# Optimization experiments

Hardware: AMD Instinct MI355X
Metric: run time of the kernel (lower is better)

The kernel has to match this reference:

```python
import jax, jax.numpy as jnp
import numpy as np

EPS = 1e-8  # smoothing_radius


def setup_inputs() -> dict:
    key = jax.random.key(0)
    ks = jax.random.split(key, 8)
    T, S, D = 2048, 1024, 3
    H, FIN, FOUT = 64, 7, 4
    return {
        "reference_length": jnp.ones((), jnp.float32),
        "source_points": jax.random.normal(ks[0], (S, D), jnp.float32),
        "target_points": jax.random.normal(ks[1], (T, D), jnp.float32),
        "source_strengths": jax.random.uniform(ks[2], (S,), jnp.float32),
        "source_area": jax.random.uniform(ks[3], (S,), jnp.float32),
        "source_normal": jax.random.normal(ks[4], (S, D), jnp.float32),
        "W1": jax.random.normal(ks[5], (FIN, H), jnp.float32) / np.sqrt(FIN),
        "b1": jnp.zeros((H,), jnp.float32),
        "W2": jax.random.normal(ks[6], (H, FOUT), jnp.float32) / np.sqrt(H),
        "b2": jnp.zeros((FOUT,), jnp.float32),
    }


def _legendre4(x):
    # First 4 Legendre polynomials P1..P4 (n_spherical_harmonics = 4)
    x2 = x * x
    p1 = x
    p2 = 0.5 * (3.0 * x2 - 1.0)
    p3 = 0.5 * (5.0 * x2 - 3.0) * x
    p4 = 0.125 * ((35.0 * x2 - 30.0) * x2 + 3.0)
    return jnp.stack([p1, p2, p3, p4], axis=-1)


def _kernel_forward(reference_length, source_points, target_points,
                    source_strengths, source_area, source_normal,
                    W1, b1, W2, b2):
    D = source_points.shape[-1]
    # Dimensionless relative positions: [T, S, D]
    r = (target_points[:, None, :] - source_points[None, :, :]) / reference_length
    r2 = jnp.sum(r * r, axis=-1) + EPS * EPS          # [T, S]
    n2 = jnp.sum(source_normal * source_normal, -1) + EPS * EPS  # [S]
    # Invariant features: source scalar, smoothed log-magnitudes, pair Legendre terms
    log_r = 0.5 * jnp.log(r2)                          # [T, S]
    log_n = 0.5 * jnp.log(n2)                          # [S]
    cos = jnp.einsum('tsd,sd->ts', r, source_normal) / jnp.sqrt(r2 * n2[None, :])
    feats = jnp.concatenate([
        jnp.broadcast_to(source_area[None, :, None], r2.shape + (1,)),
        log_r[..., None],
        jnp.broadcast_to(log_n[None, :, None], r2.shape + (1,)),
        _legendre4(cos),
    ], axis=-1)                                        # [T, S, 7]
    # MLP kernel network with tanh squashing (network_type='mlp')
    h = jax.nn.silu(feats @ W1 + b1)                   # [T, S, 64]
    out = jnp.tanh(h @ W2 + b2)                        # [T, S, 4]
    # Physical far-field decay: scalar ~ 1/r^{D-2}, vector ~ 1/r^{D-1}
    inv_r = jax.lax.rsqrt(r2)
    decay_s = inv_r ** (D - 2)
    decay_v = inv_r ** (D - 1)
    w = source_strengths[None, :]                      # [1, S]
    scalar = jnp.sum(w * decay_s * out[..., 0], axis=-1)  # [T]
    # Rotationally invariant vector reprojection: radial + 2 coeffs per non-radial vector
    r_hat = r * inv_r[..., None]
    n_hat = source_normal / jnp.sqrt(n2)[:, None]
    n_hat_b = jnp.broadcast_to(n_hat[None], r.shape)
    vec = (out[..., 1:2] * r_hat
           + out[..., 2:3] * n_hat_b
           + out[..., 3:4] * jnp.cross(r_hat, n_hat_b))  # [T, S, D]
    vector = jnp.einsum('ts,tsd->td', w * decay_v, vec)   # [T, D]
    return jnp.concatenate([scalar[:, None], vector], axis=-1)  # [T, 1+D]


def reference(reference_length, source_points, target_points, source_strengths,
              source_area, source_normal, W1, b1, W2, b2):
    return _kernel_forward(reference_length, source_points, target_points,
                           source_strengths, source_area, source_normal,
                           W1, b1, W2, b2)
```

## Files before the change

### kernel.cpp

```cpp
#include <hip/hip_runtime.h>

#define EPS2 1e-16f

constexpr int H      = 64;
constexpr int PBLOCK = 256;
constexpr int BLOCK  = 256;
constexpr int NCHUNK = 4;
constexpr float LOG2E = 1.4426950408889634f;

__device__ __forceinline__ float rcpf_fast(float x) { return __builtin_amdgcn_rcpf(x); }
__device__ __forceinline__ float rsqf_fast(float x) { return __builtin_amdgcn_rsqf(x); }
__device__ __forceinline__ float exp2_fast(float x) { return __builtin_amdgcn_exp2f(x); }

__global__ void prep(const float* __restrict__ refLenP,
                     const float* __restrict__ srcP,
                     const float* __restrict__ srcN,
                     const float* __restrict__ wgtP,
                     const float* __restrict__ areaP,
                     const float* __restrict__ W1,
                     const float* __restrict__ b1,
                     const float* __restrict__ W2,
                     float* __restrict__ ws, int S)
{
    const int nSrcBlk = (S + PBLOCK - 1) / PBLOCK;
    const int bid = blockIdx.x;
    if (bid < nSrcBlk) {
        const int s = bid * PBLOCK + threadIdx.x;
        if (s < S) {
            const float invL = rcpf_fast(refLenP[0]);
            float px = srcP[s * 3 + 0] * invL;
            float py = srcP[s * 3 + 1] * invL;
            float pz = srcP[s * 3 + 2] * invL;
            float nx = srcN[s * 3 + 0];
            float ny = srcN[s * 3 + 1];
            float nz = srcN[s * 3 + 2];
            float n2 = fmaf(nx, nx, fmaf(ny, ny, nz * nz)) + EPS2;
            float inv_n = rsqf_fast(n2);
            float l2n = __log2f(n2);
            float4* sPA = (float4*)(ws + 1024);
            float4* sNB = (float4*)(ws + 1024 + 4 * S);
            float*  sw  = ws + 1024 + 8 * S;
            sPA[s] = make_float4(px, py, pz, areaP[s]);
            sNB[s] = make_float4(nx * inv_n, ny * inv_n, nz * inv_n, l2n);
            sw[s]  = wgtP[s];
        }
    } else {
        const int h = threadIdx.x;
        if (h < H) {
            float* p = ws + h * 16;
            p[0] = -LOG2E * W1[0 * H + h];
            p[1] = -0.5f  * W1[1 * H + h];
            p[2] = -0.5f  * W1[2 * H + h];
            p[3] = -LOG2E * W1[3 * H + h];
            p[4] = -LOG2E * W1[4 * H + h];
            p[5] = -LOG2E * W1[5 * H + h];
            p[6] = -LOG2E * b1[h];
            p[7] = -LOG2E * W1[6 * H + h];
            p[8]  = -2.0f * W2[h * 4 + 0];
            p[9]  = -2.0f * W2[h * 4 + 1];
            p[10] = -2.0f * W2[h * 4 + 2];
            p[11] = -2.0f * W2[h * 4 + 3];
            p[12] = 0.f; p[13] = 0.f; p[14] = 0.f; p[15] = 0.f;
        }
    }
}

__global__ __launch_bounds__(BLOCK)
void bh_kernel(const float* __restrict__ refLenP,
               const float* __restrict__ tgtP,
               const float* __restrict__ b2,
               const float* __restrict__ ws,
               float* __restrict__ out,
               int S, int T)
{
    __shared__ float red[4][4];

    const int tid = threadIdx.x;
    const int t = blockIdx.x;

    const float invL = rcpf_fast(refLenP[0]);
    const float tx = tgtP[t * 3 + 0] * invL;
    const float ty = tgtP[t * 3 + 1] * invL;
    const float tz = tgtP[t * 3 + 2] * invL;

    const float4* __restrict__ sPA = (const float4*)(ws + 1024);
    const float4* __restrict__ sNB = (const float4*)(ws + 1024 + 4 * S);
    const float*  __restrict__ sw  = ws + 1024 + 8 * S;
    const float4* __restrict__ wq  = (const float4*)ws;

    float f1[NCHUNK], f3[NCHUNK], f4[NCHUNK], f5[NCHUNK], f6[NCHUNK];
    float fa[NCHUNK], f2s[NCHUNK];
    #pragma unroll
    for (int c = 0; c < NCHUNK; ++c) {
        const int s = tid + c * BLOCK;
        const int sc = (s < S) ? s : (S - 1);
        const float4 pa = sPA[sc];
        const float4 nb = sNB[sc];
        float rx = tx - pa.x;
        float ry = ty - pa.y;
        float rz = tz - pa.z;
        float r2 = fmaf(rx, rx, fmaf(ry, ry, fmaf(rz, rz, EPS2)));
        float ir = rsqf_fast(r2);
        f1[c] = __log2f(r2);
        float cosv = fmaf(rx, nb.x, fmaf(ry, nb.y, rz * nb.z)) * ir;
        float c2 = cosv * cosv;
        fa[c]  = pa.w;
        f2s[c] = nb.w;
        f3[c] = cosv;
        f4[c] = fmaf(c2, 1.5f, -0.5f);
        f5[c] = (c2 * 2.5f - 1.5f) * cosv;
        f6[c] = fmaf(fmaf(c2, 4.375f, -3.75f), c2, 0.375f);
    }

    float o0[NCHUNK], o1[NCHUNK], o2[NCHUNK], o3[NCHUNK];
    {
        const float s2 = 2.0f * LOG2E;
        const float b20 = s2 * b2[0], b21 = s2 * b2[1];
        const float b22 = s2 * b2[2], b23 = s2 * b2[3];
        #pragma unroll
        for (int c = 0; c < NCHUNK; ++c) {
            o0[c] = b20; o1[c] = b21; o2[c] = b22; o3[c] = b23;
        }
    }

    #pragma unroll 4
    for (int h = 0; h < H; ++h) {
        const float4 wa = wq[h * 4 + 0];
        const float4 wb = wq[h * 4 + 1];
        const float4 w2 = wq[h * 4 + 2];
        #pragma unroll
        for (int c = 0; c < NCHUNK; ++c) {
            float a = fmaf(fa[c], wa.x, fmaf(f2s[c], wa.z, wb.z));
            a = fmaf(f1[c], wa.y, a);
            a = fmaf(f3[c], wa.w, a);
            a = fmaf(f4[c], wb.x, a);
            a = fmaf(f5[c], wb.y, a);
            a = fmaf(f6[c], wb.w, a);
            float e  = exp2_fast(a);
            float sg = rcpf_fast(1.0f + e);
            float hv = a * sg;
            o0[c] = fmaf(hv, w2.x, o0[c]);
            o1[c] = fmaf(hv, w2.y, o1[c]);
            o2[c] = fmaf(hv, w2.z, o2[c]);
            o3[c] = fmaf(hv, w2.w, o3[c]);
        }
    }

    float acc0 = 0.f, acc1 = 0.f, acc2 = 0.f, acc3 = 0.f;
    #pragma unroll
    for (int c = 0; c < NCHUNK; ++c) {
        const int s = tid + c * BLOCK;
        const int sc = (s < S) ? s : (S - 1);
        const float4 pa = sPA[sc];
        const float4 nb = sNB[sc];
        const float wgt = (s < S) ? sw[sc] : 0.0f;
        float rx = tx - pa.x;
        float ry = ty - pa.y;
        float rz = tz - pa.z;
        float r2 = fmaf(rx, rx, fmaf(ry, ry, fmaf(rz, rz, EPS2)));
        float ir = rsqf_fast(r2);
        float wsv = wgt * ir;
        float wvv = wsv * ir;

        float tt[4];
        float oo[4] = {o0[c], o1[c], o2[c], o3[c]};
        #pragma unroll
        for (int k = 0; k < 4; ++k) {
            float m = fminf(fmaxf(oo[k], -126.f), 126.f);
            float E = exp2_fast(m);
            tt[k] = (E - 1.0f) * rcpf_fast(E + 1.0f);
        }

        acc0 = fmaf(wsv, tt[0], acc0);
        float rhx = rx * ir, rhy = ry * ir, rhz = rz * ir;
        float cxx = rhy * nb.z - rhz * nb.y;
        float cxy = rhz * nb.x - rhx * nb.z;
        float cxz = rhx * nb.y - rhy * nb.x;
        float vx = tt[1] * rhx + tt[2] * nb.x + tt[3] * cxx;
        float vy = tt[1] * rhy + tt[2] * nb.y + tt[3] * cxy;
        float vz = tt[1] * rhz + tt[2] * nb.z + tt[3] * cxz;
        acc1 = fmaf(wvv, vx, acc1);
        acc2 = fmaf(wvv, vy, acc2);
        acc3 = fmaf(wvv, vz, acc3);
    }

    #pragma unroll
    for (int off = 32; off > 0; off >>= 1) {
        acc0 += __shfl_down(acc0, off);
        acc1 += __shfl_down(acc1, off);
        acc2 += __shfl_down(acc2, off);
        acc3 += __shfl_down(acc3, off);
    }
    const int wave = tid >> 6;
    const int lane = tid & 63;
    if (lane == 0) {
        red[wave][0] = acc0; red[wave][1] = acc1;
        red[wave][2] = acc2; red[wave][3] = acc3;
    }
    __syncthreads();
    if (tid < 4) {
        float v = red[0][tid] + red[1][tid] + red[2][tid] + red[3][tid];
        out[t * 4 + tid] = v;
    }
}

extern "C" void kernel_launch(void* const* d_in, const int* in_sizes, int n_in,
                              void* d_out, int out_size, void* d_ws, size_t ws_size,
                              hipStream_t stream) {
    const float* refLen = (const float*)d_in[0];
    const float* srcP   = (const float*)d_in[1];
    const float* tgtP   = (const float*)d_in[2];
    const float* w      = (const float*)d_in[3];
    const float* area   = (const float*)d_in[4];
    const float* srcN   = (const float*)d_in[5];
    const float* W1     = (const float*)d_in[6];
    const float* b1     = (const float*)d_in[7];
    const float* W2     = (const float*)d_in[8];
    const float* b2     = (const float*)d_in[9];
    float* out          = (float*)d_out;
    float* ws           = (float*)d_ws;

    const int S = in_sizes[3];
    const int T = in_sizes[2] / 3;
    const int nSrcBlk = (S + PBLOCK - 1) / PBLOCK;

    prep<<<nSrcBlk + 1, PBLOCK, 0, stream>>>(refLen, srcP, srcN, w, area, W1, b1, W2, ws, S);
    bh_kernel<<<T, BLOCK, 0, stream>>>(refLen, tgtP, b2, ws, out, S, T);
}
```

Baseline: 120.7 us.

## Move per-pair MLP layers onto bf16 MFMA with LDS-staged fragments

Replaces the scalar FMA loop over 64 hidden units with two bf16 MFMA 16x16x32 stages per 16-source tile. Features are packed to bf16 in LDS, the hidden SiLU activations are written back to LDS as bf16 for the second matmul, and the outputs go through LDS before the tanh and vector reprojection step. The aim is to cut VALU FMA work on the first and last layers. In exchange, precision drops to bf16 and there is LDS round-trip traffic, while the 64 exp/rcp SiLU evaluations per pair stay on the VALU. Only a quarter of the MFMA K dimension is used, since the upper lanes are zero-padded.

```diff
diff --git a/kernel.cpp b/kernel.cpp
--- a/kernel.cpp
+++ b/kernel.cpp
@@ -1,16 +1,24 @@
 #include <hip/hip_runtime.h>
 
+typedef __attribute__((ext_vector_type(4))) float f32x4;
+typedef __attribute__((ext_vector_type(8))) short bf16x8;
+
 #define EPS2 1e-16f
-
-constexpr int H      = 64;
 constexpr int PBLOCK = 256;
 constexpr int BLOCK  = 256;
-constexpr int NCHUNK = 4;
 constexpr float LOG2E = 1.4426950408889634f;
 
-__device__ __forceinline__ float rcpf_fast(float x) { return __builtin_amdgcn_rcpf(x); }
-__device__ __forceinline__ float rsqf_fast(float x) { return __builtin_amdgcn_rsqf(x); }
-__device__ __forceinline__ float exp2_fast(float x) { return __builtin_amdgcn_exp2f(x); }
+__device__ __forceinline__ float rcpf_fast(float x){ return __builtin_amdgcn_rcpf(x); }
+__device__ __forceinline__ float rsqf_fast(float x){ return __builtin_amdgcn_rsqf(x); }
+__device__ __forceinline__ float exp2_fast(float x){ return __builtin_amdgcn_exp2f(x); }
+__device__ __forceinline__ unsigned cvt_pk_bf16(float lo, float hi){
+    unsigned d;
+    asm("v_cvt_pk_bf16_f32 %0, %1, %2" : "=v"(d) : "v"(lo), "v"(hi));
+    return d;
+}
+__device__ __forceinline__ bf16x8 as_frag(int4 v){
+    union { int4 i; bf16x8 f; } u; u.i = v; return u.f;
+}
 
 __global__ void prep(const float* __restrict__ refLenP,
                      const float* __restrict__ srcP,
@@ -28,39 +36,43 @@
         const int s = bid * PBLOCK + threadIdx.x;
         if (s < S) {
             const float invL = rcpf_fast(refLenP[0]);
-            float px = srcP[s * 3 + 0] * invL;
-            float py = srcP[s * 3 + 1] * invL;
-            float pz = srcP[s * 3 + 2] * invL;
-            float nx = srcN[s * 3 + 0];
-            float ny = srcN[s * 3 + 1];
-            float nz = srcN[s * 3 + 2];
-            float n2 = fmaf(nx, nx, fmaf(ny, ny, nz * nz)) + EPS2;
+            float px = srcP[s*3+0]*invL, py = srcP[s*3+1]*invL, pz = srcP[s*3+2]*invL;
+            float nx = srcN[s*3+0], ny = srcN[s*3+1], nz = srcN[s*3+2];
+            float n2 = fmaf(nx,nx, fmaf(ny,ny, nz*nz)) + EPS2;
             float inv_n = rsqf_fast(n2);
             float l2n = __log2f(n2);
-            float4* sPA = (float4*)(ws + 1024);
-            float4* sNB = (float4*)(ws + 1024 + 4 * S);
-            float*  sw  = ws + 1024 + 8 * S;
+            float4* sPA = (float4*)(ws + 384);
+            float4* sNB = (float4*)(ws + 384 + 4*S);
+            float*  sw  = ws + 384 + 8*S;
             sPA[s] = make_float4(px, py, pz, areaP[s]);
-            sNB[s] = make_float4(nx * inv_n, ny * inv_n, nz * inv_n, l2n);
+            sNB[s] = make_float4(nx*inv_n, ny*inv_n, nz*inv_n, l2n);
             sw[s]  = wgtP[s];
         }
     } else {
-        const int h = threadIdx.x;
-        if (h < H) {
-            float* p = ws + h * 16;
-            p[0] = -LOG2E * W1[0 * H + h];
-            p[1] = -0.5f  * W1[1 * H + h];
-            p[2] = -0.5f  * W1[2 * H + h];
-            p[3] = -LOG2E * W1[3 * H + h];
-            p[4] = -LOG2E * W1[4 * H + h];
-            p[5] = -LOG2E * W1[5 * H + h];
-            p[6] = -LOG2E * b1[h];
-            p[7] = -LOG2E * W1[6 * H + h];
-            p[8]  = -2.0f * W2[h * 4 + 0];
-            p[9]  = -2.0f * W2[h * 4 + 1];
-            p[10] = -2.0f * W2[h * 4 + 2];
-            p[11] = -2.0f * W2[h * 4 + 3];
-            p[12] = 0.f; p[13] = 0.f; p[14] = 0.f; p[15] = 0.f;
+        const int t = threadIdx.x;
+        unsigned* W1u = (unsigned*)ws;
+        unsigned* W2u = (unsigned*)ws + 256;
+        if (t < 64) {
+            const int h = t;
+            float v[8];
+            v[0] = -LOG2E * W1[0*64 + h];
+            v[1] = -0.5f  * W1[1*64 + h];
+            v[2] = -0.5f  * W1[2*64 + h];
+            v[3] = -LOG2E * W1[3*64 + h];
+            v[4] = -LOG2E * W1[4*64 + h];
+            v[5] = -LOG2E * W1[5*64 + h];
+            v[6] = -LOG2E * W1[6*64 + h];
+            v[7] = -LOG2E * b1[h];
+            #pragma unroll
+            for (int r = 0; r < 4; ++r)
+                W1u[h*4 + r] = cvt_pk_bf16(v[2*r], v[2*r+1]);
+        } else if (t < 192) {
+            const int idx = t - 64;
+            const int j = idx >> 5;
+            const int hp = idx & 31;
+            float a = -2.0f * W2[(2*hp  )*4 + j];
+            float b = -2.0f * W2[(2*hp+1)*4 + j];
+            W2u[j*32 + hp] = cvt_pk_bf16(a, b);
         }
     }
 }
@@ -73,112 +85,119 @@
                float* __restrict__ out,
                int S, int T)
 {
-    __shared__ float red[4][4];
+    __shared__ unsigned featsL[4][64][4];
+    __shared__ unsigned hvL[4][16][36];
+    __shared__ f32x4   oL[4][64];
+    __shared__ float   red[4][4];
 
     const int tid = threadIdx.x;
-    const int t = blockIdx.x;
+    const int wv  = tid >> 6;
+    const int l   = tid & 63;
+    const int col = l & 15;
+    const int q   = l >> 4;
+    const int t   = blockIdx.x;
+
+    const unsigned* __restrict__ W1u = (const unsigned*)ws;
+    const unsigned* __restrict__ W2u = (const unsigned*)ws + 256;
+    const float4* __restrict__ sPA = (const float4*)(ws + 384);
+    const float4* __restrict__ sNB = (const float4*)(ws + 384 + 4*S);
+    const float*  __restrict__ sw  = ws + 384 + 8*S;
+
+    int4 A1[4];
+    #pragma unroll
+    for (int mt = 0; mt < 4; ++mt) {
+        int4 r = *(const int4*)&W1u[(mt*16 + col) * 4];
+        A1[mt] = (q == 0) ? r : make_int4(0,0,0,0);
+    }
+    int4 A2[2];
+    #pragma unroll
+    for (int kt = 0; kt < 2; ++kt) {
+        const int rowj = col;
+        const int src = (rowj < 4) ? rowj : 0;
+        int4 r = *(const int4*)&W2u[src*32 + kt*16 + q*4];
+        A2[kt] = (rowj < 4) ? r : make_int4(0,0,0,0);
+    }
 
     const float invL = rcpf_fast(refLenP[0]);
-    const float tx = tgtP[t * 3 + 0] * invL;
-    const float ty = tgtP[t * 3 + 1] * invL;
-    const float tz = tgtP[t * 3 + 2] * invL;
-
-    const float4* __restrict__ sPA = (const float4*)(ws + 1024);
-    const float4* __restrict__ sNB = (const float4*)(ws + 1024 + 4 * S);
-    const float*  __restrict__ sw  = ws + 1024 + 8 * S;
-    const float4* __restrict__ wq  = (const float4*)ws;
-
-    float f1[NCHUNK], f3[NCHUNK], f4[NCHUNK], f5[NCHUNK], f6[NCHUNK];
-    float fa[NCHUNK], f2s[NCHUNK];
-    #pragma unroll
-    for (int c = 0; c < NCHUNK; ++c) {
-        const int s = tid + c * BLOCK;
-        const int sc = (s < S) ? s : (S - 1);
+    const float tx = tgtP[t*3+0]*invL;
+    const float ty = tgtP[t*3+1]*invL;
+    const float tz = tgtP[t*3+2]*invL;
+    const float s2 = 2.0f * LOG2E;
+    const f32x4 b2init = { s2*b2[0], s2*b2[1], s2*b2[2], s2*b2[3] };
+    const f32x4 zero4  = { 0.f, 0.f, 0.f, 0.f };
+
+    float acc0 = 0.f, acc1 = 0.f, acc2 = 0.f, acc3 = 0.f;
+
+    for (int it = 0; it < 4; ++it) {
+        const int s  = wv*256 + it*64 + l;
+        const int sc = (s < S) ? s : 0;
         const float4 pa = sPA[sc];
         const float4 nb = sNB[sc];
-        float rx = tx - pa.x;
-        float ry = ty - pa.y;
-        float rz = tz - pa.z;
-        float r2 = fmaf(rx, rx, fmaf(ry, ry, fmaf(rz, rz, EPS2)));
+        const float wgt = (s < S) ? sw[sc] : 0.f;
+
+        float rx = tx - pa.x, ry = ty - pa.y, rz = tz - pa.z;
+        float r2 = fmaf(rx,rx, fmaf(ry,ry, fmaf(rz,rz, EPS2)));
         float ir = rsqf_fast(r2);
-        f1[c] = __log2f(r2);
-        float cosv = fmaf(rx, nb.x, fmaf(ry, nb.y, rz * nb.z)) * ir;
+        float l2r = __log2f(r2);
+        float cosv = fmaf(rx,nb.x, fmaf(ry,nb.y, rz*nb.z)) * ir;
         float c2 = cosv * cosv;
-        fa[c]  = pa.w;
-        f2s[c] = nb.w;
-        f3[c] = cosv;
-        f4[c] = fmaf(c2, 1.5f, -0.5f);
-        f5[c] = (c2 * 2.5f - 1.5f) * cosv;
-        f6[c] = fmaf(fmaf(c2, 4.375f, -3.75f), c2, 0.375f);
-    }
-
-    float o0[NCHUNK], o1[NCHUNK], o2[NCHUNK], o3[NCHUNK];
-    {
-        const float s2 = 2.0f * LOG2E;
-        const float b20 = s2 * b2[0], b21 = s2 * b2[1];
-        const float b22 = s2 * b2[2], b23 = s2 * b2[3];
+        float P2 = fmaf(c2, 1.5f, -0.5f);
+        float P3 = (c2*2.5f - 1.5f) * cosv;
+        float P4 = fmaf(fmaf(c2, 4.375f, -3.75f), c2, 0.375f);
+        unsigned f01 = cvt_pk_bf16(pa.w, l2r);
+        unsigned f23 = cvt_pk_bf16(nb.w, cosv);
+        unsigned f45 = cvt_pk_bf16(P2,   P3);
+        unsigned f67 = cvt_pk_bf16(P4,   1.0f);
+        *(int4*)&featsL[wv][l][0] = make_int4((int)f01, (int)f23, (int)f45, (int)f67);
+
         #pragma unroll
-        for (int c = 0; c < NCHUNK; ++c) {
-            o0[c] = b20; o1[c] = b21; o2[c] = b22; o3[c] = b23;
-        }
-    }
-
-    #pragma unroll 4
-    for (int h = 0; h < H; ++h) {
-        const float4 wa = wq[h * 4 + 0];
-        const float4 wb = wq[h * 4 + 1];
-        const float4 w2 = wq[h * 4 + 2];
+        for (int pb = 0; pb < 4; ++pb) {
+            int4 braw = *(const int4*)&featsL[wv][pb*16 + col][0];
+            int4 b1i = (q == 0) ? braw : make_int4(0,0,0,0);
+            bf16x8 B1 = as_frag(b1i);
+
+            #pragma unroll
+            for (int mt = 0; mt < 4; ++mt) {
+                f32x4 c1 = __builtin_amdgcn_mfma_f32_16x16x32_bf16(
+                               as_frag(A1[mt]), B1, zero4, 0, 0, 0);
+                float hv0, hv1, hv2, hv3;
+                { float e = exp2_fast(c1[0]); hv0 = c1[0] * rcpf_fast(1.0f + e); }
+                { float e = exp2_fast(c1[1]); hv1 = c1[1] * rcpf_fast(1.0f + e); }
+                { float e = exp2_fast(c1[2]); hv2 = c1[2] * rcpf_fast(1.0f + e); }
+                { float e = exp2_fast(c1[3]); hv3 = c1[3] * rcpf_fast(1.0f + e); }
+                unsigned h01 = cvt_pk_bf16(hv0, hv1);
+                unsigned h23 = cvt_pk_bf16(hv2, hv3);
+                *(uint2*)&hvL[wv][col][mt*8 + q*2] = make_uint2(h01, h23);
+            }
+
+            f32x4 oacc = b2init;
+            #pragma unroll
+            for (int kt = 0; kt < 2; ++kt) {
+                int4 b2raw = *(const int4*)&hvL[wv][col][kt*16 + q*4];
+                oacc = __builtin_amdgcn_mfma_f32_16x16x32_bf16(
+                           as_frag(A2[kt]), as_frag(b2raw), oacc, 0, 0, 0);
+            }
+            if (q == 0) oL[wv][pb*16 + col] = oacc;
+        }
+
+        f32x4 ov = oL[wv][l];
+        float tt[4];
         #pragma unroll
-        for (int c = 0; c < NCHUNK; ++c) {
-            float a = fmaf(fa[c], wa.x, fmaf(f2s[c], wa.z, wb.z));
-            a = fmaf(f1[c], wa.y, a);
-            a = fmaf(f3[c], wa.w, a);
-            a = fmaf(f4[c], wb.x, a);
-            a = fmaf(f5[c], wb.y, a);
-            a = fmaf(f6[c], wb.w, a);
-            float e  = exp2_fast(a);
-            float sg = rcpf_fast(1.0f + e);
-            float hv = a * sg;
-            o0[c] = fmaf(hv, w2.x, o0[c]);
-            o1[c] = fmaf(hv, w2.y, o1[c]);
-            o2[c] = fmaf(hv, w2.z, o2[c]);
-            o3[c] = fmaf(hv, w2.w, o3[c]);
-        }
-    }
-
-    float acc0 = 0.f, acc1 = 0.f, acc2 = 0.f, acc3 = 0.f;
-    #pragma unroll
-    for (int c = 0; c < NCHUNK; ++c) {
-        const int s = tid + c * BLOCK;
-        const int sc = (s < S) ? s : (S - 1);
-        const float4 pa = sPA[sc];
-        const float4 nb = sNB[sc];
-        const float wgt = (s < S) ? sw[sc] : 0.0f;
-        float rx = tx - pa.x;
-        float ry = ty - pa.y;
-        float rz = tz - pa.z;
-        float r2 = fmaf(rx, rx, fmaf(ry, ry, fmaf(rz, rz, EPS2)));
-        float ir = rsqf_fast(r2);
+        for (int k = 0; k < 4; ++k) {
+            float m = fminf(fmaxf(ov[k], -126.f), 126.f);
+            float E = exp2_fast(m);
+            tt[k] = (E - 1.0f) * rcpf_fast(E + 1.0f);
+        }
         float wsv = wgt * ir;
         float wvv = wsv * ir;
-
-        float tt[4];
-        float oo[4] = {o0[c], o1[c], o2[c], o3[c]};
-        #pragma unroll
-        for (int k = 0; k < 4; ++k) {
-            float m = fminf(fmaxf(oo[k], -126.f), 126.f);
-            float E = exp2_fast(m);
-            tt[k] = (E - 1.0f) * rcpf_fast(E + 1.0f);
-        }
-
         acc0 = fmaf(wsv, tt[0], acc0);
-        float rhx = rx * ir, rhy = ry * ir, rhz = rz * ir;
-        float cxx = rhy * nb.z - rhz * nb.y;
-        float cxy = rhz * nb.x - rhx * nb.z;
-        float cxz = rhx * nb.y - rhy * nb.x;
-        float vx = tt[1] * rhx + tt[2] * nb.x + tt[3] * cxx;
-        float vy = tt[1] * rhy + tt[2] * nb.y + tt[3] * cxy;
-        float vz = tt[1] * rhz + tt[2] * nb.z + tt[3] * cxz;
+        float rhx = rx*ir, rhy = ry*ir, rhz = rz*ir;
+        float cxx = rhy*nb.z - rhz*nb.y;
+        float cxy = rhz*nb.x - rhx*nb.z;
+        float cxz = rhx*nb.y - rhy*nb.x;
+        float vx = tt[1]*rhx + tt[2]*nb.x + tt[3]*cxx;
+        float vy = tt[1]*rhy + tt[2]*nb.y + tt[3]*cxy;
+        float vz = tt[1]*rhz + tt[2]*nb.z + tt[3]*cxz;
         acc1 = fmaf(wvv, vx, acc1);
         acc2 = fmaf(wvv, vy, acc2);
         acc3 = fmaf(wvv, vz, acc3);
@@ -191,16 +210,14 @@
         acc2 += __shfl_down(acc2, off);
         acc3 += __shfl_down(acc3, off);
     }
-    const int wave = tid >> 6;
-    const int lane = tid & 63;
-    if (lane == 0) {
-        red[wave][0] = acc0; red[wave][1] = acc1;
-        red[wave][2] = acc2; red[wave][3] = acc3;
+    if ((tid & 63) == 0) {
+        red[wv][0] = acc0; red[wv][1] = acc1;
+        red[wv][2] = acc2; red[wv][3] = acc3;
     }
     __syncthreads();
     if (tid < 4) {
         float v = red[0][tid] + red[1][tid] + red[2][tid] + red[3][tid];
-        out[t * 4 + tid] = v;
+        out[t*4 + tid] = v;
     }
 }
 
```

Measured after the change: 110.2 us. -8.7%, faster.
